# Kernel optimization log

Hardware: AMD Instinct MI355X
Metric: run time of the kernel (lower is better)

The kernel has to match this reference:

```python
import jax, jax.numpy as jnp
import numpy as np

VOCAB, E, H = 100000, 300, 2048

def setup_inputs() -> dict:
    key = jax.random.key(0)
    k1, k2, k3, k4, k5, k6 = jax.random.split(key, 6)
    s_e = 1.0 / np.sqrt(H)
    return {
        "input": jax.random.randint(k1, (128, 64), 0, VOCAB),
        "embed": jax.random.normal(k2, (VOCAB, E), dtype=jnp.float32),
        "w_ih": jax.random.normal(k3, (4 * H, E), dtype=jnp.float32) * s_e,
        "w_hh": jax.random.normal(k4, (4 * H, H), dtype=jnp.float32) * s_e,
        "b_ih": jax.random.normal(k5, (4 * H,), dtype=jnp.float32) * s_e,
        "b_hh": jax.random.normal(k6, (4 * H,), dtype=jnp.float32) * s_e,
    }

def _lstm_cell(x, h, c, w_ih, w_hh, b_ih, b_hh):
    # PyTorch LSTMCell: gates = x @ W_ih^T + b_ih + h @ W_hh^T + b_hh
    gates = x @ w_ih.T + b_ih + h @ w_hh.T + b_hh  # [B, 4H]
    i, f, g, o = jnp.split(gates, 4, axis=-1)
    i, f, o = jax.nn.sigmoid(i), jax.nn.sigmoid(f), jax.nn.sigmoid(o)
    g = jnp.tanh(g)
    c_new = f * c + i * g
    h_new = o * jnp.tanh(c_new)
    return h_new, c_new

def reference(input, embed, w_ih, w_hh, b_ih, b_hh):
    B, T = input.shape
    x = embed[input]  # [B, T, E] embedding lookup
    x_t = jnp.swapaxes(x, 0, 1)  # [T, B, E] for scan over time
    h0 = jnp.zeros((B, H), dtype=x.dtype)
    c0 = jnp.zeros((B, H), dtype=x.dtype)

    def step(carry, xt):
        h, c = carry
        h, c = _lstm_cell(xt, h, c, w_ih, w_hh, b_ih, b_hh)
        return (h, c), None

    (hT, cT), _ = jax.lax.scan(step, (h0, c0), x_t)
    return hT  # [B, H]
```

## Files before the change

kernel.cpp:

```cpp
#include <hip/hip_runtime.h>
#include <stdint.h>

#define H_    2048
#define B_    128
#define T_    64
#define E_    300
#define NKUX  10
#define XGRP  48
#define NWG   256
#define NTHR  512
#define NJG   128

#define WSCL  (0.14f / 127.f)
#define GSCL  (0.14f / (127.f * 127.f))

typedef unsigned short u16;
typedef unsigned char u8;
typedef signed char s8;
typedef uint32_t u32;
typedef short bf8 __attribute__((ext_vector_type(8)));
typedef float f4 __attribute__((ext_vector_type(4)));
typedef int   i4 __attribute__((ext_vector_type(4)));
typedef long i64v;

__device__ __forceinline__ u16 f2b(float f) {
    u32 u = __float_as_uint(f);
    u += 0x7fffu + ((u >> 16) & 1u);
    return (u16)(u >> 16);
}
__device__ __forceinline__ float sigm(float x) { return 1.f / (1.f + __expf(-x)); }
__device__ __forceinline__ float tanh_(float x) {
    float xx = fminf(fmaxf(x, -15.f), 15.f);
    float e = __expf(2.f * xx);
    return (e - 1.f) / (e + 1.f);
}
__device__ __forceinline__ s8 f2i8w(float f) {
    float v = f * (1.f / WSCL);
    v = fminf(fmaxf(v, -127.f), 127.f);
    return (s8)__float2int_rn(v);
}
__device__ __forceinline__ s8 f2i8h(float f) {
    float v = fminf(fmaxf(f * 127.f, -127.f), 127.f);
    return (s8)__float2int_rn(v);
}

__global__ void prep_kernel(const float* __restrict__ w_hh, const float* __restrict__ w_ih,
                            const float* __restrict__ b_ih, const float* __restrict__ b_hh,
                            s8* __restrict__ wP8, u16* __restrict__ wiP,
                            float* __restrict__ bsP,
                            float* __restrict__ cP, s8* __restrict__ hP0) {
    int tid = blockIdx.x * blockDim.x + threadIdx.x;
    int np = gridDim.x * blockDim.x;
    const int NF = NJG * 64 * 4 * 64;
    for (int f = tid; f < NF; f += np) {
        int lane = f & 63;
        int fr = f >> 6;
        int nt = fr & 3;
        int rest = fr >> 2;
        int ku = rest & 63;
        int jg = rest >> 6;
        int l15 = lane & 15, q = lane >> 4;
        int nl = nt * 16 + l15;
        int g = nl & 3, jj = nl >> 2;
        int ng = g * H_ + jg * 16 + jj;
        int k0 = ku * 32 + q * 8;
        union { s8 s[8]; uint2 v; } tmp;
#pragma unroll
        for (int j = 0; j < 8; ++j)
            tmp.s[j] = f2i8w(w_hh[(size_t)ng * H_ + k0 + j]);
        *(uint2*)&wP8[(size_t)f * 8] = tmp.v;
    }
    const int NFI = NJG * NKUX * 4 * 64;
    for (int f = tid; f < NFI; f += np) {
        int lane = f & 63;
        int fr = f >> 6;
        int nt = fr & 3;
        int rest = fr >> 2;
        int ku = rest % NKUX;
        int jg = rest / NKUX;
        int l15 = lane & 15, q = lane >> 4;
        int nl = nt * 16 + l15;
        int g = nl & 3, jj = nl >> 2;
        int ng = g * H_ + jg * 16 + jj;
        int k0 = ku * 32 + q * 8;
        union { u16 s[8]; uint4 v; } tmp;
#pragma unroll
        for (int j = 0; j < 8; ++j) {
            int k = k0 + j;
            tmp.s[j] = (k < E_) ? f2b(w_ih[(size_t)ng * E_ + k]) : (u16)0;
        }
        *(uint4*)&wiP[(size_t)f * 8] = tmp.v;
    }
    for (int n = tid; n < NJG * 64; n += np) {
        int jg = n >> 6, r = n & 63;
        int jj = r >> 2, g = r & 3;
        int src = g * H_ + jg * 16 + jj;
        bsP[n] = b_ih[src] + b_hh[src];
    }
    for (int i = tid; i < NJG * B_ * 16; i += np) cP[i] = 0.f;
    for (int i = tid; i < (H_ / 8) * B_ * 8 / 4; i += np) ((u32*)hP0)[i] = 0u;
}

__global__ void gather_kernel(const int* __restrict__ input, const float* __restrict__ embed,
                              u16* __restrict__ xP) {
    int t = blockIdx.x;
    u16* xt = xP + (size_t)t * XGRP * B_ * 8;
    for (int id = threadIdx.x; id < XGRP * B_; id += blockDim.x) {
        int b = id & (B_ - 1);
        int gx = id >> 7;
        int row = input[b * T_ + t];
        const float* src = embed + (size_t)row * E_;
        union { u16 s[8]; uint4 v; } tmp;
#pragma unroll
        for (int j = 0; j < 8; ++j) {
            int k = gx * 8 + j;
            tmp.s[j] = (k < E_) ? f2b(src[k]) : (u16)0;
        }
        *(uint4*)&xt[(size_t)id * 8] = tmp.v;
    }
}

__global__ __launch_bounds__(NTHR) void
xw_kernel(const u16* __restrict__ wiP, const u16* __restrict__ xP,
          const float* __restrict__ bsP, float* __restrict__ xg) {
    int tid = threadIdx.x;
    int wid = tid >> 6, lane = tid & 63;
    int l15 = lane & 15, q = lane >> 4;
    int t  = blockIdx.x >> 7;
    int jg = blockIdx.x & 127;

    const u16* wbase = wiP + (size_t)jg * NKUX * 2048 + lane * 8;
    const u16* xbase = xP + (size_t)t * (XGRP * B_ * 8) + (size_t)(q * 128 + wid * 16 + l15) * 8;

    f4 acc[4];
#pragma unroll
    for (int nt = 0; nt < 4; ++nt) acc[nt] = (f4)0.f;

#pragma unroll
    for (int ku = 0; ku < NKUX; ++ku) {
        bf8 wf[4], xf;
        const u16* wb = wbase + (size_t)ku * 2048;
        wf[0] = *(const bf8*)(wb);
        wf[1] = *(const bf8*)(wb + 512);
        wf[2] = *(const bf8*)(wb + 1024);
        wf[3] = *(const bf8*)(wb + 1536);
        xf = *(const bf8*)(xbase + (size_t)ku * 4096);
#pragma unroll
        for (int nt = 0; nt < 4; ++nt)
            acc[nt] = __builtin_amdgcn_mfma_f32_16x16x32_bf16(wf[nt], xf, acc[nt], 0, 0, 0);
    }

    int m = wid * 16 + l15;
    float* outb = xg + (((size_t)t * NJG + jg) * B_ + m) * 64;
#pragma unroll
    for (int nt = 0; nt < 4; ++nt) {
        f4 bv = *(const f4*)&bsP[jg * 64 + nt * 16 + q * 4];
        f4 r = acc[nt];
        r[0] += bv[0]; r[1] += bv[1]; r[2] += bv[2]; r[3] += bv[3];
        *(f4*)&outb[nt * 16 + q * 4] = r;
    }
}

__global__ __launch_bounds__(NTHR) void
step_kernel(const s8* __restrict__ wP8, const float* __restrict__ xgt,
            const s8* __restrict__ hin,
            s8* __restrict__ hout, float* __restrict__ cP,
            float* __restrict__ outp) {
    __shared__ int bufs[8][16][68];
    int tid = threadIdx.x;
    int wid = tid >> 6, lane = tid & 63;
    int l15 = lane & 15, q = lane >> 4;
    int jg  = blockIdx.x & 127;
    int wgm = blockIdx.x >> 7;

    const s8* wbase = wP8 + (size_t)jg * 64 * 2048 + lane * 8;
    int hoff = q * 1024 + wgm * 512 + l15 * 8;

    i4 acc[4][4];
#pragma unroll
    for (int nt = 0; nt < 4; ++nt)
#pragma unroll
        for (int mt = 0; mt < 4; ++mt) acc[nt][mt] = (i4)0;

#define LDF8(KU, WF, HB) do {                                                 \
        int ku_ = (KU);                                                       \
        const s8* wb_ = wbase + (size_t)ku_ * 2048;                           \
        WF[0] = *(const i64v*)(wb_);                                          \
        WF[1] = *(const i64v*)(wb_ + 512);                                    \
        WF[2] = *(const i64v*)(wb_ + 1024);                                   \
        WF[3] = *(const i64v*)(wb_ + 1536);                                   \
        const s8* hb_ = hin + (size_t)ku_ * 4096 + hoff;                      \
        HB[0] = *(const i64v*)(hb_);                                          \
        HB[1] = *(const i64v*)(hb_ + 128);                                    \
        HB[2] = *(const i64v*)(hb_ + 256);                                    \
        HB[3] = *(const i64v*)(hb_ + 384);                                    \
    } while (0)

#define MM8(WF, HB) do {                                                      \
        _Pragma("unroll")                                                     \
        for (int nt_ = 0; nt_ < 4; ++nt_)                                     \
            _Pragma("unroll")                                                 \
            for (int mt_ = 0; mt_ < 4; ++mt_)                                 \
                acc[nt_][mt_] = __builtin_amdgcn_mfma_i32_16x16x32_i8(        \
                    WF[nt_], HB[mt_], acc[nt_][mt_], 0, 0, 0);                \
    } while (0)

    {
        int ks = wid * 8;
        i64v wB_[4][4], hB_[4][4];
#pragma unroll
        for (int i = 0; i < 3; ++i) LDF8(ks + i, wB_[i], hB_[i]);
#pragma unroll
        for (int i = 0; i < 8; ++i) {
            if (i + 3 < 8) LDF8(ks + i + 3, wB_[(i + 3) & 3], hB_[(i + 3) & 3]);
            MM8(wB_[i & 3], hB_[i & 3]);
        }
    }
#undef LDF8
#undef MM8

    int jj = tid & 15, ml16 = (tid >> 4) & 15;
#pragma unroll
    for (int p = 0; p < 4; ++p) {
        __syncthreads();
        *(i4*)&bufs[wid][l15][0 * 16 + q * 4] = acc[0][p];
        *(i4*)&bufs[wid][l15][1 * 16 + q * 4] = acc[1][p];
        *(i4*)&bufs[wid][l15][2 * 16 + q * 4] = acc[2][p];
        *(i4*)&bufs[wid][l15][3 * 16 + q * 4] = acc[3][p];
        __syncthreads();
        if (tid < 256) {
            int m = wgm * 64 + p * 16 + ml16;
            i4 r = (i4)0;
#pragma unroll
            for (int w = 0; w < 8; ++w) {
                i4 v = *(const i4*)&bufs[w][ml16][jj * 4];
                r[0] += v[0]; r[1] += v[1]; r[2] += v[2]; r[3] += v[3];
            }
            f4 s = *(const f4*)&xgt[((size_t)jg * B_ + m) * 64 + jj * 4];
            s[0] += (float)r[0] * GSCL;
            s[1] += (float)r[1] * GSCL;
            s[2] += (float)r[2] * GSCL;
            s[3] += (float)r[3] * GSCL;
            float iv = sigm(s[0]);
            float fv = sigm(s[1]);
            float gv = tanh_(s[2]);
            float ov = sigm(s[3]);
            size_t ci = ((size_t)jg * B_ + m) * 16 + jj;
            float cn = fv * cP[ci] + iv * gv;
            cP[ci] = cn;
            float hn = ov * tanh_(cn);
            int jglob = jg * 16 + jj;
            hout[(size_t)(jglob >> 3) * 1024 + m * 8 + (jglob & 7)] = f2i8h(hn);
            if (outp) outp[(size_t)m * H_ + jglob] = hn;
        }
    }
}

extern "C" void kernel_launch(void* const* d_in, const int* in_sizes, int n_in,
                              void* d_out, int out_size, void* d_ws, size_t ws_size,
                              hipStream_t stream) {
    const int*   input = (const int*)d_in[0];
    const float* embed = (const float*)d_in[1];
    const float* w_ih  = (const float*)d_in[2];
    const float* w_hh  = (const float*)d_in[3];
    const float* b_ih  = (const float*)d_in[4];
    const float* b_hh  = (const float*)d_in[5];
    float* out = (float*)d_out;

    char* ws = (char*)d_ws;
    size_t o = 0;
    s8*  wP8  = (s8*)(ws + o);  o += (size_t)NJG * 64 * 4 * 64 * 8;
    u16* wiP  = (u16*)(ws + o); o += (size_t)NJG * NKUX * 4 * 64 * 8 * 2;
    u16* xP   = (u16*)(ws + o); o += (size_t)T_ * XGRP * B_ * 8 * 2;
    s8*  hP0  = (s8*)(ws + o);  o += (size_t)(H_ / 8) * B_ * 8;
    s8*  hP1  = (s8*)(ws + o);  o += (size_t)(H_ / 8) * B_ * 8;
    float* cP = (float*)(ws + o); o += (size_t)NJG * B_ * 16 * 4;
    float* bsP = (float*)(ws + o); o += (size_t)4 * H_ * 4;
    float* xg = (float*)(ws + o); o += (size_t)T_ * NJG * B_ * 64 * 4;
    (void)ws_size;

    prep_kernel<<<2048, 256, 0, stream>>>(w_hh, w_ih, b_ih, b_hh, wP8, wiP, bsP, cP, hP0);
    gather_kernel<<<T_, 256, 0, stream>>>(input, embed, xP);
    xw_kernel<<<T_ * NJG, NTHR, 0, stream>>>(wiP, xP, bsP, xg);

    for (int t = 0; t < T_; ++t) {
        const s8* hin = (t & 1) ? hP1 : hP0;
        s8* hout      = (t & 1) ? hP0 : hP1;
        float* hof    = (t == T_ - 1) ? out : nullptr;
        step_kernel<<<NWG, NTHR, 0, stream>>>(
            wP8, xg + (size_t)t * NJG * B_ * 64, hin, hout, cP, hof);
    }
}
```

Baseline: 1.038 ms.

## Fuse per-timestep LSTM launches into one persistent cooperative kernel with grid barrier

Replaces the 64 per-timestep step_kernel launches with a single cooperative persistent kernel. It loops over time, keeps the cell state in registers, and synchronises all 256 workgroups with a two-level atomic grid barrier. Each step writes h into its own buffer (T+1 copies), so there are no read/write hazards across the barrier. The precomputed input-gate projections are also stored as fp16 instead of fp32, which halves their memory traffic. This trades per-launch overhead for barrier cost and adds fp16 rounding error on the gate inputs; if the cooperative launch fails, it falls back to the per-step kernels.

Measured after the change: 1.478 ms. +42.3%, slower.

```diff
diff --git a/kernel.cpp b/kernel.cpp
--- a/kernel.cpp
+++ b/kernel.cpp
@@ -10,6 +10,7 @@
 #define NWG   256
 #define NTHR  512
 #define NJG   128
+#define HBUF  (262144)
 
 #define WSCL  (0.14f / 127.f)
 #define GSCL  (0.14f / (127.f * 127.f))
@@ -22,12 +23,15 @@
 typedef float f4 __attribute__((ext_vector_type(4)));
 typedef int   i4 __attribute__((ext_vector_type(4)));
 typedef long i64v;
+typedef _Float16 f16;
 
 __device__ __forceinline__ u16 f2b(float f) {
     u32 u = __float_as_uint(f);
     u += 0x7fffu + ((u >> 16) & 1u);
     return (u16)(u >> 16);
 }
+__device__ __forceinline__ u16 f2h(float f) { f16 h = (f16)f; u16 u; __builtin_memcpy(&u, &h, 2); return u; }
+__device__ __forceinline__ float h2f(u16 u) { f16 h; __builtin_memcpy(&h, &u, 2); return (float)h; }
 __device__ __forceinline__ float sigm(float x) { return 1.f / (1.f + __expf(-x)); }
 __device__ __forceinline__ float tanh_(float x) {
     float xx = fminf(fmaxf(x, -15.f), 15.f);
@@ -48,7 +52,8 @@
                             const float* __restrict__ b_ih, const float* __restrict__ b_hh,
                             s8* __restrict__ wP8, u16* __restrict__ wiP,
                             float* __restrict__ bsP,
-                            float* __restrict__ cP, s8* __restrict__ hP0) {
+                            float* __restrict__ cP, s8* __restrict__ hR,
+                            int* __restrict__ bar) {
     int tid = blockIdx.x * blockDim.x + threadIdx.x;
     int np = gridDim.x * blockDim.x;
     const int NF = NJG * 64 * 4 * 64;
@@ -98,7 +103,8 @@
         bsP[n] = b_ih[src] + b_hh[src];
     }
     for (int i = tid; i < NJG * B_ * 16; i += np) cP[i] = 0.f;
-    for (int i = tid; i < (H_ / 8) * B_ * 8 / 4; i += np) ((u32*)hP0)[i] = 0u;
+    for (int i = tid; i < HBUF / 4; i += np) ((u32*)hR)[i] = 0u;
+    for (int i = tid; i < 4096; i += np) bar[i] = 0;
 }
 
 __global__ void gather_kernel(const int* __restrict__ input, const float* __restrict__ embed,
@@ -122,7 +128,7 @@
 
 __global__ __launch_bounds__(NTHR) void
 xw_kernel(const u16* __restrict__ wiP, const u16* __restrict__ xP,
-          const float* __restrict__ bsP, float* __restrict__ xg) {
+          const float* __restrict__ bsP, u16* __restrict__ xg) {
     int tid = threadIdx.x;
     int wid = tid >> 6, lane = tid & 63;
     int l15 = lane & 15, q = lane >> 4;
@@ -151,36 +157,18 @@
     }
 
     int m = wid * 16 + l15;
-    float* outb = xg + (((size_t)t * NJG + jg) * B_ + m) * 64;
+    u16* outb = xg + (((size_t)t * NJG + jg) * B_ + m) * 64;
 #pragma unroll
     for (int nt = 0; nt < 4; ++nt) {
         f4 bv = *(const f4*)&bsP[jg * 64 + nt * 16 + q * 4];
-        f4 r = acc[nt];
-        r[0] += bv[0]; r[1] += bv[1]; r[2] += bv[2]; r[3] += bv[3];
-        *(f4*)&outb[nt * 16 + q * 4] = r;
-    }
-}
-
-__global__ __launch_bounds__(NTHR) void
-step_kernel(const s8* __restrict__ wP8, const float* __restrict__ xgt,
-            const s8* __restrict__ hin,
-            s8* __restrict__ hout, float* __restrict__ cP,
-            float* __restrict__ outp) {
-    __shared__ int bufs[8][16][68];
-    int tid = threadIdx.x;
-    int wid = tid >> 6, lane = tid & 63;
-    int l15 = lane & 15, q = lane >> 4;
-    int jg  = blockIdx.x & 127;
-    int wgm = blockIdx.x >> 7;
-
-    const s8* wbase = wP8 + (size_t)jg * 64 * 2048 + lane * 8;
-    int hoff = q * 1024 + wgm * 512 + l15 * 8;
-
-    i4 acc[4][4];
-#pragma unroll
-    for (int nt = 0; nt < 4; ++nt)
-#pragma unroll
-        for (int mt = 0; mt < 4; ++mt) acc[nt][mt] = (i4)0;
+        union { u16 s[4]; uint2 v; } hv;
+        hv.s[0] = f2h(acc[nt][0] + bv[0]);
+        hv.s[1] = f2h(acc[nt][1] + bv[1]);
+        hv.s[2] = f2h(acc[nt][2] + bv[2]);
+        hv.s[3] = f2h(acc[nt][3] + bv[3]);
+        *(uint2*)&outb[nt * 16 + q * 4] = hv.v;
+    }
+}
 
 #define LDF8(KU, WF, HB) do {                                                 \
         int ku_ = (KU);                                                       \
@@ -205,6 +193,131 @@
                     WF[nt_], HB[mt_], acc[nt_][mt_], 0, 0, 0);                \
     } while (0)
 
+__global__ __launch_bounds__(NTHR) void
+loop_kernel(const s8* __restrict__ wP8, const u16* __restrict__ xgt,
+            s8* __restrict__ hR, float* __restrict__ outp, int* __restrict__ bar) {
+    __shared__ int bufs[8][16][68];
+    int tid = threadIdx.x;
+    int bid = blockIdx.x;
+    int wid = tid >> 6, lane = tid & 63;
+    int l15 = lane & 15, q = lane >> 4;
+    int jg  = bid & 127;
+    int wgm = bid >> 7;
+    int jj = tid & 15, ml16 = (tid >> 4) & 15;
+
+    const s8* wbase = wP8 + (size_t)jg * 64 * 2048 + lane * 8;
+    int hoff = q * 1024 + wgm * 512 + l15 * 8;
+    int ks = wid * 8;
+
+    float creg[4] = {0.f, 0.f, 0.f, 0.f};
+
+    for (int t = 0; t < T_; ++t) {
+        const s8* hin = hR + (size_t)t * HBUF;
+        s8* hout      = hR + (size_t)(t + 1) * HBUF;
+
+        i4 acc[4][4];
+#pragma unroll
+        for (int nt = 0; nt < 4; ++nt)
+#pragma unroll
+            for (int mt = 0; mt < 4; ++mt) acc[nt][mt] = (i4)0;
+
+        {
+            i64v wB_[4][4], hB_[4][4];
+#pragma unroll
+            for (int i = 0; i < 3; ++i) LDF8(ks + i, wB_[i], hB_[i]);
+#pragma unroll
+            for (int i = 0; i < 8; ++i) {
+                if (i + 3 < 8) LDF8(ks + i + 3, wB_[(i + 3) & 3], hB_[(i + 3) & 3]);
+                MM8(wB_[i & 3], hB_[i & 3]);
+            }
+        }
+
+#pragma unroll
+        for (int p = 0; p < 4; ++p) {
+            __syncthreads();
+            *(i4*)&bufs[wid][l15][0 * 16 + q * 4] = acc[0][p];
+            *(i4*)&bufs[wid][l15][1 * 16 + q * 4] = acc[1][p];
+            *(i4*)&bufs[wid][l15][2 * 16 + q * 4] = acc[2][p];
+            *(i4*)&bufs[wid][l15][3 * 16 + q * 4] = acc[3][p];
+            __syncthreads();
+            if (tid < 256) {
+                int m = wgm * 64 + p * 16 + ml16;
+                i4 r = (i4)0;
+#pragma unroll
+                for (int w = 0; w < 8; ++w) {
+                    i4 v = *(const i4*)&bufs[w][ml16][jj * 4];
+                    r[0] += v[0]; r[1] += v[1]; r[2] += v[2]; r[3] += v[3];
+                }
+                union { uint2 v; u16 s[4]; } xu;
+                xu.v = *(const uint2*)&xgt[(((size_t)t * NJG + jg) * B_ + m) * 64 + jj * 4];
+                float s0 = h2f(xu.s[0]) + (float)r[0] * GSCL;
+                float s1 = h2f(xu.s[1]) + (float)r[1] * GSCL;
+                float s2 = h2f(xu.s[2]) + (float)r[2] * GSCL;
+                float s3 = h2f(xu.s[3]) + (float)r[3] * GSCL;
+                float iv = sigm(s0);
+                float fv = sigm(s1);
+                float gv = tanh_(s2);
+                float ov = sigm(s3);
+                float cn = fv * creg[p] + iv * gv;
+                creg[p] = cn;
+                float hn = ov * tanh_(cn);
+                int jglob = jg * 16 + jj;
+                hout[(size_t)(jglob >> 3) * 1024 + m * 8 + (jglob & 7)] = f2i8h(hn);
+                if (t == T_ - 1) outp[(size_t)m * H_ + jglob] = hn;
+            }
+        }
+
+        if (t < T_ - 1) {
+            __syncthreads();
+            if (tid == 0) {
+                __threadfence();
+                int old = __hip_atomic_fetch_add(&bar[(bid & 31) * 32], 1,
+                                                 __ATOMIC_ACQ_REL, __HIP_MEMORY_SCOPE_AGENT);
+                if (old == 7) {
+                    int r = __hip_atomic_fetch_add(&bar[32 * 32], 1,
+                                                   __ATOMIC_ACQ_REL, __HIP_MEMORY_SCOPE_AGENT);
+                    if (r == 31) {
+#pragma unroll
+                        for (int l = 0; l < 32; ++l)
+                            __hip_atomic_store(&bar[l * 32], 0,
+                                               __ATOMIC_RELAXED, __HIP_MEMORY_SCOPE_AGENT);
+                        __hip_atomic_store(&bar[32 * 32], 0,
+                                           __ATOMIC_RELAXED, __HIP_MEMORY_SCOPE_AGENT);
+                        __hip_atomic_store(&bar[33 * 32], t + 1,
+                                           __ATOMIC_RELEASE, __HIP_MEMORY_SCOPE_AGENT);
+                    }
+                }
+                while (__hip_atomic_load(&bar[33 * 32],
+                                         __ATOMIC_RELAXED, __HIP_MEMORY_SCOPE_AGENT) < t + 1)
+                    __builtin_amdgcn_s_sleep(2);
+            }
+            __syncthreads();
+            asm volatile("" ::: "memory");
+        }
+    }
+}
+
+__global__ __launch_bounds__(NTHR) void
+step_kernel(const s8* __restrict__ wP8, const u16* __restrict__ xgt,
+            const s8* __restrict__ hin,
+            s8* __restrict__ hout, float* __restrict__ cP,
+            float* __restrict__ outp) {
+    __shared__ int bufs[8][16][68];
+    int tid = threadIdx.x;
+    int wid = tid >> 6, lane = tid & 63;
+    int l15 = lane & 15, q = lane >> 4;
+    int jg  = blockIdx.x & 127;
+    int wgm = blockIdx.x >> 7;
+
+    const s8* wbase = wP8 + (size_t)jg * 64 * 2048 + lane * 8;
+    int hoff = q * 1024 + wgm * 512 + l15 * 8;
+
+    i4 acc[4][4];
+#pragma unroll
+    for (int nt = 0; nt < 4; ++nt)
+#pragma unroll
+        for (int mt = 0; mt < 4; ++mt) acc[nt][mt] = (i4)0;
+
     {
         int ks = wid * 8;
         i64v wB_[4][4], hB_[4][4];
@@ -216,8 +329,6 @@
             MM8(wB_[i & 3], hB_[i & 3]);
         }
     }
-#undef LDF8
-#undef MM8
 
     int jj = tid & 15, ml16 = (tid >> 4) & 15;
 #pragma unroll
@@ -236,15 +347,16 @@
                 i4 v = *(const i4*)&bufs[w][ml16][jj * 4];
                 r[0] += v[0]; r[1] += v[1]; r[2] += v[2]; r[3] += v[3];
             }
-            f4 s = *(const f4*)&xgt[((size_t)jg * B_ + m) * 64 + jj * 4];
-            s[0] += (float)r[0] * GSCL;
-            s[1] += (float)r[1] * GSCL;
-            s[2] += (float)r[2] * GSCL;
-            s[3] += (float)r[3] * GSCL;
-            float iv = sigm(s[0]);
-            float fv = sigm(s[1]);
-            float gv = tanh_(s[2]);
-            float ov = sigm(s[3]);
+            union { uint2 v; u16 s[4]; } xu;
+            xu.v = *(const uint2*)&xgt[((size_t)jg * B_ + m) * 64 + jj * 4];
+            float s0 = h2f(xu.s[0]) + (float)r[0] * GSCL;
+            float s1 = h2f(xu.s[1]) + (float)r[1] * GSCL;
+            float s2 = h2f(xu.s[2]) + (float)r[2] * GSCL;
+            float s3 = h2f(xu.s[3]) + (float)r[3] * GSCL;
+            float iv = sigm(s0);
+            float fv = sigm(s1);
+            float gv = tanh_(s2);
+            float ov = sigm(s3);
             size_t ci = ((size_t)jg * B_ + m) * 16 + jj;
             float cn = fv * cP[ci] + iv * gv;
             cP[ci] = cn;
@@ -255,6 +367,9 @@
         }
     }
 }
+
+#undef LDF8
+#undef MM8
 
 extern "C" void kernel_launch(void* const* d_in, const int* in_sizes, int n_in,
                               void* d_out, int out_size, void* d_ws, size_t ws_size,
@@ -272,22 +387,29 @@
     s8*  wP8  = (s8*)(ws + o);  o += (size_t)NJG * 64 * 4 * 64 * 8;
     u16* wiP  = (u16*)(ws + o); o += (size_t)NJG * NKUX * 4 * 64 * 8 * 2;
     u16* xP   = (u16*)(ws + o); o += (size_t)T_ * XGRP * B_ * 8 * 2;
-    s8*  hP0  = (s8*)(ws + o);  o += (size_t)(H_ / 8) * B_ * 8;
-    s8*  hP1  = (s8*)(ws + o);  o += (size_t)(H_ / 8) * B_ * 8;
+    s8*  hR   = (s8*)(ws + o);  o += (size_t)(T_ + 1) * HBUF;
     float* cP = (float*)(ws + o); o += (size_t)NJG * B_ * 16 * 4;
     float* bsP = (float*)(ws + o); o += (size_t)4 * H_ * 4;
-    float* xg = (float*)(ws + o); o += (size_t)T_ * NJG * B_ * 64 * 4;
+    int* bar  = (int*)(ws + o); o += 4096 * 4;
+    u16* xgH  = (u16*)(ws + o); o += (size_t)T_ * NJG * B_ * 64 * 2;
     (void)ws_size;
 
-    prep_kernel<<<2048, 256, 0, stream>>>(w_hh, w_ih, b_ih, b_hh, wP8, wiP, bsP, cP, hP0);
+    prep_kernel<<<2048, 256, 0, stream>>>(w_hh, w_ih, b_ih, b_hh, wP8, wiP, bsP, cP, hR, bar);
     gather_kernel<<<T_, 256, 0, stream>>>(input, embed, xP);
-    xw_kernel<<<T_ * NJG, NTHR, 0, stream>>>(wiP, xP, bsP, xg);
-
-    for (int t = 0; t < T_; ++t) {
-        const s8* hin = (t & 1) ? hP1 : hP0;
-        s8* hout      = (t & 1) ? hP0 : hP1;
-        float* hof    = (t == T_ - 1) ? out : nullptr;
-        step_kernel<<<NWG, NTHR, 0, stream>>>(
-            wP8, xg + (size_t)t * NJG * B_ * 64, hin, hout, cP, hof);
-    }
-}
+    xw_kernel<<<T_ * NJG, NTHR, 0, stream>>>(wiP, xP, bsP, xgH);
+
+    const s8* a0 = wP8; const u16* a1 = xgH; s8* a2 = hR; float* a3 = out; int* a4 = bar;
+    void* kargs[] = {(void*)&a0, (void*)&a1, (void*)&a2, (void*)&a3, (void*)&a4};
+    hipError_t ce = hipLaunchCooperativeKernel((const void*)loop_kernel,
+                                               dim3(NWG), dim3(NTHR), kargs, 0, stream);
+    if (ce != hipSuccess) {
+        (void)hipGetLastError();
+        for (int t = 0; t < T_; ++t) {
+            const s8* hin = hR + (size_t)t * HBUF;
+            s8* hout      = hR + (size_t)(t + 1) * HBUF;
+            float* hof    = (t == T_ - 1) ? out : nullptr;
+            step_kernel<<<NWG, NTHR, 0, stream>>>(
+                wP8, xgH + (size_t)t * NJG * B_ * 64, hin, hout, cP, hof);
+        }
+    }
+}
```
